# Optimization experiments

Measured on AMD Instinct MI355X. Metric: run time of the kernel, lower is better.

Reference implementation:

```python
import jax, jax.numpy as jnp
import numpy as np
import math

DIM = 512
HEADS = 8
DIM_HEAD = DIM // HEADS
TIME_DIM = 512
EPS = 1e-5


def _ln(x, g, b):
    m = jnp.mean(x, axis=-1, keepdims=True)
    v = jnp.var(x, axis=-1, keepdims=True)
    return (x - m) * jax.lax.rsqrt(v + EPS) * g + b


def setup_inputs() -> dict:
    key = jax.random.key(0)
    ks = jax.random.split(key, 16)
    s = 0.02
    return {
        "con_features": jax.random.normal(ks[0], (4, 1024, DIM), jnp.float32),
        "diff_features": jax.random.normal(ks[1], (4, 1024, DIM), jnp.float32),
        "time_emb": jax.random.normal(ks[2], (4, TIME_DIM), jnp.float32),
        "ln_con_g": jnp.ones((DIM,), jnp.float32),
        "ln_con_b": jnp.zeros((DIM,), jnp.float32),
        "ln_diff_g": jnp.ones((DIM,), jnp.float32),
        "ln_diff_b": jnp.zeros((DIM,), jnp.float32),
        "wq": jax.random.normal(ks[3], (DIM, DIM), jnp.float32) * s,
        "wk": jax.random.normal(ks[4], (DIM, DIM), jnp.float32) * s,
        "wv": jax.random.normal(ks[5], (DIM, DIM), jnp.float32) * s,
        "w_out": jax.random.normal(ks[6], (DIM, DIM), jnp.float32) * s,
        "b_out": jnp.zeros((DIM,), jnp.float32),
        "w_emd1": jax.random.normal(ks[7], (TIME_DIM, 2 * DIM), jnp.float32) * s,
        "b_emd1": jnp.zeros((2 * DIM,), jnp.float32),
        "w_emd2": jax.random.normal(ks[8], (2 * DIM, 2 * DIM), jnp.float32) * s,
        "b_emd2": jnp.zeros((2 * DIM,), jnp.float32),
        "mlp_ln_g": jnp.ones((DIM,), jnp.float32),
        "mlp_ln_b": jnp.zeros((DIM,), jnp.float32),
        "mlp_w1": jax.random.normal(ks[9], (DIM, DIM), jnp.float32) * s,
        "mlp_b1": jnp.zeros((DIM,), jnp.float32),
        "mlp_w2": jax.random.normal(ks[10], (DIM, DIM), jnp.float32) * s,
        "mlp_b2": jnp.zeros((DIM,), jnp.float32),
    }


def reference(con_features, diff_features, time_emb,
              ln_con_g, ln_con_b, ln_diff_g, ln_diff_b,
              wq, wk, wv, w_out, b_out,
              w_emd1, b_emd1, w_emd2, b_emd2,
              mlp_ln_g, mlp_ln_b, mlp_w1, mlp_b1, mlp_w2, mlp_b2):
    b, n, _ = diff_features.shape
    fea_q = _ln(diff_features, ln_diff_g, ln_diff_b)
    fea_kv = _ln(con_features, ln_con_g, ln_con_b)
    # projections (no bias) + split heads: b n (h d) -> b h n d
    def heads(x):
        return x.reshape(b, n, HEADS, DIM_HEAD).transpose(0, 2, 1, 3)
    q = heads(fea_q @ wq)
    k = heads(fea_kv @ wk)
    v = heads(fea_kv @ wv)
    # 2D FFT over (n, d), ortho norm
    qf = jnp.fft.fft2(q, axes=(-2, -1), norm="ortho")
    kf = jnp.fft.fft2(k, axes=(-2, -1), norm="ortho")
    dots = jnp.einsum("bhnd,bhmd->bhnm", qf, jnp.conj(kf))  # q @ k^H
    attn_c = jnp.fft.ifft2(dots, axes=(-2, -1), norm="ortho")
    mag = jnp.sqrt(attn_c.real ** 2 + attn_c.imag ** 2)
    attn = jax.nn.softmax(mag, axis=-1) / math.sqrt(DIM_HEAD)
    out = jnp.einsum("bhnm,bhmd->bhnd", attn, v)
    out = out.transpose(0, 2, 1, 3).reshape(b, n, DIM)  # b h n d -> b n (h d)
    # global per-sample normalization over (n, dim); torch.std uses ddof=1
    mu = jnp.mean(out, axis=(-2, -1), keepdims=True)
    sd = jnp.std(out, axis=(-2, -1), keepdims=True, ddof=1)
    out1 = (out - mu) / sd
    # FiLM from time embedding
    t = jax.nn.silu(time_emb @ w_emd1 + b_emd1)
    t = t @ w_emd2 + b_emd2
    mean_t, std_t = jnp.split(t, 2, axis=-1)
    out1 = out1 * std_t[:, None, :] + mean_t[:, None, :]
    out1 = out1 @ w_out + b_out
    # FeedForward: LN -> Linear -> GELU(exact) -> Linear
    h = _ln(out1, mlp_ln_g, mlp_ln_b)
    h = jax.nn.gelu(h @ mlp_w1 + mlp_b1, approximate=False)
    return h @ mlp_w2 + mlp_b2
```

## Files before the change

kernel.cpp:

```cpp
#include <hip/hip_runtime.h>
#include <math.h>


typedef _Float16 f16;
typedef _Float16 f16x8 __attribute__((ext_vector_type(8)));
typedef float f32x4 __attribute__((ext_vector_type(4)));

#define ROWS 4096
#define NTOK 1024
#define NB   4
#define NH   8
#define DH   64

__device__ __forceinline__ void glds16(const f16* g, f16* l) {
    __builtin_amdgcn_global_load_lds((const __attribute__((address_space(1))) void*)g,
                                     (__attribute__((address_space(3))) void*)l, 16, 0, 0);
}

struct PrepArgs { const float* src[6]; f16* dst[6]; };

__global__ __launch_bounds__(256) void k_prep(PrepArgs pa, float* stats,
                                              const float* b_emd1, const float* b_emd2,
                                              float* tbacc, float* filmp) {
    __shared__ float tile[32][33];
    int m = blockIdx.z;
    const float* src = pa.src[m];
    f16* dst = pa.dst[m];
    int i0 = blockIdx.y * 32;
    int o0 = blockIdx.x * 32;
    for (int r = threadIdx.y; r < 32; r += 8)
        tile[r][threadIdx.x] = src[(i0 + r) * 512 + o0 + threadIdx.x];
    __syncthreads();
    for (int r = threadIdx.y; r < 32; r += 8)
        dst[(o0 + r) * 512 + i0 + threadIdx.x] = (f16)tile[threadIdx.x][r];
    if (m == 0 && blockIdx.x == 0 && blockIdx.y == 0 && threadIdx.y == 0 && threadIdx.x < 8)
        stats[threadIdx.x] = 0.f;
    if (m == 0 && blockIdx.y == 1) {
        int o = blockIdx.x * 256 + threadIdx.y * 32 + threadIdx.x;
        tbacc[o] = b_emd1[o & 1023];
        filmp[o] = b_emd2[o & 1023];
    }
}

__global__ __launch_bounds__(256) void k_ln(const float* __restrict__ x0, const float* __restrict__ g0,
                                            const float* __restrict__ b0, f16* __restrict__ o0,
                                            const float* __restrict__ x1, const float* __restrict__ g1,
                                            const float* __restrict__ b1, f16* __restrict__ o1,
                                            int n0) {
    int wid = threadIdx.x >> 6, lane = threadIdx.x & 63;
    long row = (long)blockIdx.x * 4 + wid;
    const float *x, *g, *bb; f16* o;
    if (row < n0) { x = x0 + row * 512; g = g0; bb = b0; o = o0 + row * 512; }
    else { long r = row - n0; x = x1 + r * 512; g = g1; bb = b1; o = o1 + r * 512; }
    float v[8]; float s = 0.f;
#pragma unroll
    for (int j = 0; j < 8; j++) { v[j] = x[lane + 64 * j]; s += v[j]; }
#pragma unroll
    for (int d = 32; d >= 1; d >>= 1) s += __shfl_xor(s, d, 64);
    float mean = s * (1.f / 512.f);
    float q = 0.f;
#pragma unroll
    for (int j = 0; j < 8; j++) { float t = v[j] - mean; q += t * t; }
#pragma unroll
    for (int d = 32; d >= 1; d >>= 1) q += __shfl_xor(q, d, 64);
    float inv = rsqrtf(q * (1.f / 512.f) + 1e-5f);
#pragma unroll
    for (int j = 0; j < 8; j++) {
        int c = lane + 64 * j;
        o[c] = (f16)((v[j] - mean) * inv * g[c] + bb[c]);
    }
}

__global__ __launch_bounds__(256) void k_film1s(const float* __restrict__ temb, const float* __restrict__ w1,
                                                float* __restrict__ tbacc) {
    __shared__ float tsh[4][32];
    int tid = threadIdx.x;
    int c = blockIdx.x * 256 + tid;
    int k0 = blockIdx.y * 32;
    if (tid < 128) tsh[tid >> 5][tid & 31] = temb[(tid >> 5) * 512 + k0 + (tid & 31)];
    __syncthreads();
    float a0 = 0.f, a1 = 0.f, a2 = 0.f, a3 = 0.f;
#pragma unroll 8
    for (int k = 0; k < 32; k++) {
        float w = w1[(k0 + k) * 1024 + c];
        a0 += tsh[0][k] * w; a1 += tsh[1][k] * w; a2 += tsh[2][k] * w; a3 += tsh[3][k] * w;
    }
    atomicAdd(&tbacc[c], a0);        atomicAdd(&tbacc[1024 + c], a1);
    atomicAdd(&tbacc[2048 + c], a2); atomicAdd(&tbacc[3072 + c], a3);
}

__global__ __launch_bounds__(256) void k_film2s(const float* __restrict__ tbacc, const float* __restrict__ w2,
                                                float* __restrict__ filmp) {
    __shared__ float tsh[4][32];
    int tid = threadIdx.x;
    int c = blockIdx.x * 256 + tid;
    int k0 = blockIdx.y * 32;
    if (tid < 128) {
        float v = tbacc[(tid >> 5) * 1024 + k0 + (tid & 31)];
        tsh[tid >> 5][tid & 31] = v / (1.f + __expf(-v));
    }
    __syncthreads();
    float a0 = 0.f, a1 = 0.f, a2 = 0.f, a3 = 0.f;
#pragma unroll 8
    for (int k = 0; k < 32; k++) {
        float w = w2[(k0 + k) * 1024 + c];
        a0 += tsh[0][k] * w; a1 += tsh[1][k] * w; a2 += tsh[2][k] * w; a3 += tsh[3][k] * w;
    }
    atomicAdd(&filmp[c], a0);        atomicAdd(&filmp[1024 + c], a1);
    atomicAdd(&filmp[2048 + c], a2); atomicAdd(&filmp[3072 + c], a3);
}

__global__ __launch_bounds__(256) void k_qkv(const f16* __restrict__ A16, const f16* __restrict__ C16,
                                             const f16* __restrict__ wqT, const f16* __restrict__ wkT,
                                             const f16* __restrict__ wvT,
                                             f16* __restrict__ Qh, f16* __restrict__ Kf, f16* __restrict__ Vt) {
    __shared__ __attribute__((aligned(16))) f16 sh[128 * 128 + 64 * 128];
    f16* Ash = sh;
    f16* Bsh = sh + 128 * 128;
    const int z = blockIdx.z;
    const f16* A  = (z == 0) ? A16 : C16;
    const f16* BT = (z == 0) ? wqT : (z == 1) ? wkT : wvT;
    const int tid = threadIdx.x;
    const int lane = tid & 63, wid = tid >> 6;
    const int quad = lane >> 4, l15 = lane & 15;
    const int m0 = blockIdx.x * 128, n0 = blockIdx.y * 64;
    const int wm = (wid >> 1) * 64, wn = (wid & 1) * 32;
    const int srow = lane >> 4, slot = lane & 15;
    f32x4 acc[4][2] = {};
    for (int kk = 0; kk < 512; kk += 128) {
        if (kk) __syncthreads();
#pragma unroll
        for (int c = 0; c < 8; c++) {
            int r = c * 16 + 4 * wid + srow;
            int j = slot ^ (r & 7);
            glds16(&A[(long)(m0 + r) * 512 + kk + 8 * j], &Ash[(c * 16 + 4 * wid) * 128]);
        }
#pragma unroll
        for (int c = 0; c < 4; c++) {
            int r = c * 16 + 4 * wid + srow;
            int j = slot ^ (r & 7);
            glds16(&BT[(long)(n0 + r) * 512 + kk + 8 * j], &Bsh[(c * 16 + 4 * wid) * 128]);
        }
        __syncthreads();
#pragma unroll
        for (int ks = 0; ks < 4; ks++) {
            const int rslot = ((ks * 4 + quad) ^ (l15 & 7)) * 8;
            f16x8 af[4], bf[2];
#pragma unroll
            for (int t = 0; t < 4; t++)
                af[t] = *(const f16x8*)&Ash[(wm + t * 16 + l15) * 128 + rslot];
#pragma unroll
            for (int t = 0; t < 2; t++)
                bf[t] = *(const f16x8*)&Bsh[(wn + t * 16 + l15) * 128 + rslot];
#pragma unroll
            for (int mt = 0; mt < 4; mt++)
#pragma unroll
                for (int nt = 0; nt < 2; nt++)
                    acc[mt][nt] = __builtin_amdgcn_mfma_f32_16x16x32_f16(af[mt], bf[nt], acc[mt][nt], 0, 0, 0);
        }
    }
    __syncthreads();
    const int bb = m0 >> 10, nn0 = m0 & 1023, h = blockIdx.y;
    if (z <= 1) {
#pragma unroll
        for (int mt = 0; mt < 4; mt++)
#pragma unroll
            for (int nt = 0; nt < 2; nt++)
#pragma unroll
                for (int r = 0; r < 4; r++)
                    sh[(wm + mt * 16 + quad * 4 + r) * 72 + wn + nt * 16 + l15] = (f16)acc[mt][nt][r];
        __syncthreads();
        f16* dst = (z == 0) ? Qh : Kf;
        long basebh = ((long)(bb * NH + h)) * NTOK * DH;
#pragma unroll
        for (int q2 = 0; q2 < 4; q2++) {
            int c = tid + q2 * 256;
            int row = c >> 3, col = (c & 7) * 8;
            int n = nn0 + row;
            int nr = (z == 1) ? ((NTOK - n) & (NTOK - 1)) : n;
            *(f16x8*)&dst[basebh + (long)nr * DH + col] = *(const f16x8*)&sh[row * 72 + col];
        }
    } else {
#pragma unroll
        for (int mt = 0; mt < 4; mt++)
#pragma unroll
            for (int nt = 0; nt < 2; nt++)
#pragma unroll
                for (int r = 0; r < 4; r++)
                    sh[(wn + nt * 16 + l15) * 136 + wm + mt * 16 + quad * 4 + r] = (f16)acc[mt][nt][r];
        __syncthreads();
        long basev = ((long)(bb * NH + h)) * DH * NTOK;
#pragma unroll
        for (int q2 = 0; q2 < 4; q2++) {
            int c = tid + q2 * 256;
            int d = c >> 4, col = (c & 15) * 8;
            *(f16x8*)&Vt[basev + (long)d * NTOK + nn0 + col] = *(const f16x8*)&sh[d * 136 + col];
        }
    }
}

template <int EPI>
__global__ __launch_bounds__(256) void k_gemm64(const f16* __restrict__ A, const f16* __restrict__ BT,
                                                const float* __restrict__ bias, void* __restrict__ dstv) {
    __shared__ __attribute__((aligned(16))) f16 Ash[64 * 128];
    __shared__ __attribute__((aligned(16))) f16 Bsh[64 * 128];
    const int tid = threadIdx.x;
    const int lane = tid & 63, wid = tid >> 6;
    const int quad = lane >> 4, l15 = lane & 15;
    const int m0 = blockIdx.x * 64, n0 = blockIdx.y * 64;
    const int wm = (wid >> 1) * 32, wn = (wid & 1) * 32;
    const int srow = lane >> 4, slot = lane & 15;
    f32x4 acc[2][2] = {};
    for (int kk = 0; kk < 512; kk += 128) {
        if (kk) __syncthreads();
#pragma unroll
        for (int c = 0; c < 4; c++) {
            int r = c * 16 + 4 * wid + srow;
            int j = slot ^ (r & 7);
            glds16(&A[(long)(m0 + r) * 512 + kk + 8 * j], &Ash[(c * 16 + 4 * wid) * 128]);
            glds16(&BT[(long)(n0 + r) * 512 + kk + 8 * j], &Bsh[(c * 16 + 4 * wid) * 128]);
        }
        __syncthreads();
#pragma unroll
        for (int ks = 0; ks < 4; ks++) {
            const int rslot = ((ks * 4 + quad) ^ (l15 & 7)) * 8;
            f16x8 af[2], bf[2];
#pragma unroll
            for (int t = 0; t < 2; t++) {
                af[t] = *(const f16x8*)&Ash[(wm + t * 16 + l15) * 128 + rslot];
                bf[t] = *(const f16x8*)&Bsh[(wn + t * 16 + l15) * 128 + rslot];
            }
#pragma unroll
            for (int mt = 0; mt < 2; mt++)
#pragma unroll
                for (int nt = 0; nt < 2; nt++)
                    acc[mt][nt] = __builtin_amdgcn_mfma_f32_16x16x32_f16(af[mt], bf[nt], acc[mt][nt], 0, 0, 0);
        }
    }
#pragma unroll
    for (int mt = 0; mt < 2; mt++)
#pragma unroll
        for (int nt = 0; nt < 2; nt++)
#pragma unroll
            for (int r = 0; r < 4; r++) {
                int gm = m0 + wm + mt * 16 + quad * 4 + r;
                int gn = n0 + wn + nt * 16 + l15;
                float v = acc[mt][nt][r];
                if (EPI == 3) {
                    float x = v + bias[gn];
                    ((f16*)dstv)[(long)gm * 512 + gn] = (f16)(0.5f * x * (1.0f + erff(x * 0.70710678f)));
                } else {
                    ((float*)dstv)[(long)gm * 512 + gn] = v + bias[gn];
                }
            }
}

__global__ __launch_bounds__(256) void k_attn(const f16* __restrict__ Q, const f16* __restrict__ Kf,
                                              const f16* __restrict__ Vt, float* __restrict__ out,
                                              float* __restrict__ stats) {
    __shared__ __attribute__((aligned(16))) f16 Ksh[128 * 64];
    __shared__ __attribute__((aligned(16))) f16 Vsh[80 * 128];
    __shared__ __attribute__((aligned(16))) f16 Psh[4 * 16 * 136];
    __shared__ float rbuf[8];
    const int tid = threadIdx.x, lane = tid & 63, wid = tid >> 6;
    const int quad = lane >> 4, l15 = lane & 15;
    const int bh = blockIdx.x;
    const int b = bh >> 3, h = bh & 7, q0 = blockIdx.y * 64;
    const f16* Qbh = Q + (long)bh * NTOK * DH;
    const f16* Kbh = Kf + (long)bh * NTOK * DH;
    const f16* Vbh = Vt + (long)bh * DH * NTOK;
    const int rl = lane >> 3, jj8 = (lane & 7) ^ rl;
    const int rl4 = lane >> 4, jjv = (lane & 15) ^ (4 * wid + rl4);
    for (int i = tid; i < 16 * 128; i += 256) {
        int r = i >> 7, c2 = i & 127;
        Vsh[(64 + r) * 128 + c2] = (f16)((r == 0) ? 1.f : 0.f);
    }
    const int qrow = q0 + wid * 16 + l15;
    f16x8 qf[2];
    qf[0] = *(const f16x8*)&Qbh[(long)qrow * DH + quad * 8];
    qf[1] = *(const f16x8*)&Qbh[(long)qrow * DH + 32 + quad * 8];
    f32x4 O[5] = {};

    for (int k0 = 0; k0 < NTOK; k0 += 128) {
        if (k0) __syncthreads();
#pragma unroll
        for (int c = 0; c < 4; c++) {
            int rk = c * 32 + 8 * wid + rl;
            glds16(&Kbh[(long)(k0 + rk) * DH + 8 * jj8], &Ksh[(c * 32 + 8 * wid) * 64]);
        }
#pragma unroll
        for (int c = 0; c < 4; c++) {
            int rv = c * 16 + 4 * wid + rl4;
            glds16(&Vbh[(long)rv * NTOK + k0 + 8 * jjv], &Vsh[(c * 16 + 4 * wid) * 128]);
        }
        __syncthreads();
        f32x4 S[8] = {};
#pragma unroll
        for (int ks = 0; ks < 2; ks++) {
            const int slot = ((ks * 4 + quad) ^ (l15 & 7)) * 8;
#pragma unroll
            for (int nt = 0; nt < 8; nt++) {
                f16x8 kf = *(const f16x8*)&Ksh[(nt * 16 + l15) * 64 + slot];
                S[nt] = __builtin_amdgcn_mfma_f32_16x16x32_f16(qf[ks], kf, S[nt], 0, 0, 0);
            }
        }
#pragma unroll
        for (int nt = 0; nt < 8; nt++)
#pragma unroll
            for (int r = 0; r < 4; r++) {
                float p = __expf(fminf(fabsf(S[nt][r]) - 8.f, 11.f));
                Psh[(wid * 16 + quad * 4 + r) * 136 + nt * 16 + l15] = (f16)p;
            }
#pragma unroll
        for (int ks = 0; ks < 4; ks++) {
            f16x8 pf = *(const f16x8*)&Psh[(wid * 16 + l15) * 136 + ks * 32 + quad * 8];
            const int vslot = ((ks * 4 + quad) ^ l15) * 8;
#pragma unroll
            for (int vt = 0; vt < 5; vt++) {
                f16x8 vf = *(const f16x8*)&Vsh[(vt * 16 + l15) * 128 + vslot];
                O[vt] = __builtin_amdgcn_mfma_f32_16x16x32_f16(pf, vf, O[vt], 0, 0, 0);
            }
        }
    }
    float lb[4];
#pragma unroll
    for (int r = 0; r < 4; r++) lb[r] = 0.125f / __shfl(O[4][r], lane & 48, 64);
    float lsum = 0.f, lsq = 0.f;
#pragma unroll
    for (int t = 0; t < 4; t++)
#pragma unroll
        for (int r = 0; r < 4; r++) {
            float v = O[t][r] * lb[r];
            int gn = q0 + wid * 16 + quad * 4 + r;
            int gc = h * DH + t * 16 + l15;
            out[((long)b * NTOK + gn) * 512 + gc] = v;
            lsum += v; lsq += v * v;
        }
#pragma unroll
    for (int d = 32; d >= 1; d >>= 1) { lsum += __shfl_xor(lsum, d, 64); lsq += __shfl_xor(lsq, d, 64); }
    if (lane == 0) { rbuf[wid] = lsum; rbuf[4 + wid] = lsq; }
    __syncthreads();
    if (tid == 0) {
        atomicAdd(&stats[b * 2], rbuf[0] + rbuf[1] + rbuf[2] + rbuf[3]);
        atomicAdd(&stats[b * 2 + 1], rbuf[4] + rbuf[5] + rbuf[6] + rbuf[7]);
    }
}

__global__ __launch_bounds__(256) void k_film_apply(const float* __restrict__ ao, const float* __restrict__ stats,
                                                    const float* __restrict__ filmp, f16* __restrict__ x2) {
    long base = ((long)blockIdx.x * 256 + threadIdx.x) * 4;
    int b = (int)(base >> 19);
    float sum = stats[b * 2], sq = stats[b * 2 + 1];
    const float M = 524288.f;
    float mu = sum / M;
    float var = (sq - sum * mu) / (M - 1.f);
    float isd = rsqrtf(var);
    int c = (int)(base & 511);
    float4 v = *(const float4*)&ao[base];
    float mt[4], st[4];
#pragma unroll
    for (int j = 0; j < 4; j++) { mt[j] = filmp[b * 1024 + c + j]; st[j] = filmp[b * 1024 + 512 + c + j]; }
    x2[base + 0] = (f16)(((v.x - mu) * isd) * st[0] + mt[0]);
    x2[base + 1] = (f16)(((v.y - mu) * isd) * st[1] + mt[1]);
    x2[base + 2] = (f16)(((v.z - mu) * isd) * st[2] + mt[2]);
    x2[base + 3] = (f16)(((v.w - mu) * isd) * st[3] + mt[3]);
}

extern "C" void kernel_launch(void* const* d_in, const int* in_sizes, int n_in,
                              void* d_out, int out_size, void* d_ws, size_t ws_size,
                              hipStream_t stream) {
    const float* con      = (const float*)d_in[0];
    const float* diff     = (const float*)d_in[1];
    const float* temb     = (const float*)d_in[2];
    const float* ln_con_g = (const float*)d_in[3];
    const float* ln_con_b = (const float*)d_in[4];
    const float* ln_dif_g = (const float*)d_in[5];
    const float* ln_dif_b = (const float*)d_in[6];
    const float* wq       = (const float*)d_in[7];
    const float* wk       = (const float*)d_in[8];
    const float* wv       = (const float*)d_in[9];
    const float* w_out    = (const float*)d_in[10];
    const float* b_out    = (const float*)d_in[11];
    const float* w_emd1   = (const float*)d_in[12];
    const float* b_emd1   = (const float*)d_in[13];
    const float* w_emd2   = (const float*)d_in[14];
    const float* b_emd2   = (const float*)d_in[15];
    const float* mlp_ln_g = (const float*)d_in[16];
    const float* mlp_ln_b = (const float*)d_in[17];
    const float* mlp_w1   = (const float*)d_in[18];
    const float* mlp_b1   = (const float*)d_in[19];
    const float* mlp_w2   = (const float*)d_in[20];
    const float* mlp_b2   = (const float*)d_in[21];
    float* outp = (float*)d_out;

    char* ws = (char*)d_ws;
    size_t off = 0;
    auto alloc = [&](size_t bytes) { void* p = ws + off; off += (bytes + 255) & ~(size_t)255; return p; };
    f16*   A16   = (f16*)alloc((size_t)ROWS * 512 * 2);
    f16*   C16   = (f16*)alloc((size_t)ROWS * 512 * 2);
    f16*   Qh    = (f16*)alloc((size_t)ROWS * 512 * 2);
    f16*   Kf    = (f16*)alloc((size_t)ROWS * 512 * 2);
    f16*   Vt    = (f16*)alloc((size_t)ROWS * 512 * 2);
    float* aout  = (float*)alloc((size_t)ROWS * 512 * 4);
    f16*   wqT   = (f16*)alloc(512 * 512 * 2);
    f16*   wkT   = (f16*)alloc(512 * 512 * 2);
    f16*   wvT   = (f16*)alloc(512 * 512 * 2);
    f16*   woT   = (f16*)alloc(512 * 512 * 2);
    f16*   w1T   = (f16*)alloc(512 * 512 * 2);
    f16*   w2T   = (f16*)alloc(512 * 512 * 2);
    float* tbacc = (float*)alloc(4 * 1024 * 4);
    float* filmp = (float*)alloc(4 * 1024 * 4);
    float* stats = (float*)alloc(256);
    float* out1  = (float*)Qh;
    f16*   X2    = Vt;
    f16*   X3    = A16;
    f16*   X4    = C16;

    PrepArgs pa;
    pa.src[0] = wq;  pa.src[1] = wk;  pa.src[2] = wv;
    pa.src[3] = w_out; pa.src[4] = mlp_w1; pa.src[5] = mlp_w2;
    pa.dst[0] = wqT; pa.dst[1] = wkT; pa.dst[2] = wvT;
    pa.dst[3] = woT; pa.dst[4] = w1T; pa.dst[5] = w2T;

    k_prep<<<dim3(16, 16, 6), dim3(32, 8), 0, stream>>>(pa, stats, b_emd1, b_emd2, tbacc, filmp);
    k_film1s<<<dim3(4, 16), dim3(256), 0, stream>>>(temb, w_emd1, tbacc);
    k_film2s<<<dim3(4, 32), dim3(256), 0, stream>>>(tbacc, w_emd2, filmp);
    k_ln<<<dim3(2048), dim3(256), 0, stream>>>(diff, ln_dif_g, ln_dif_b, A16,
                                               con, ln_con_g, ln_con_b, C16, ROWS);
    k_qkv<<<dim3(32, 8, 3), dim3(256), 0, stream>>>(A16, C16, wqT, wkT, wvT, Qh, Kf, Vt);
    k_attn<<<dim3(32, 16), dim3(256), 0, stream>>>(Qh, Kf, Vt, aout, stats);
    k_film_apply<<<dim3(2048), dim3(256), 0, stream>>>(aout, stats, filmp, X2);
    k_gemm64<2><<<dim3(64, 8), dim3(256), 0, stream>>>(X2, woT, b_out, (void*)out1);
    k_ln<<<dim3(1024), dim3(256), 0, stream>>>(out1, mlp_ln_g, mlp_ln_b, X3,
                                               out1, mlp_ln_g, mlp_ln_b, X3, ROWS);
    k_gemm64<3><<<dim3(64, 8), dim3(256), 0, stream>>>(X3, w1T, mlp_b1, (void*)X4);
    k_gemm64<4><<<dim3(64, 8), dim3(256), 0, stream>>>(X4, w2T, mlp_b2, (void*)outp);
}
```

Baseline: 191.8 us.

## Merge prep, LN, FiLM and QKV launches; compute softmax row sums in registers

Four pre-attention launches (weight transpose, two FiLM GEMV stages, layernorm) are folded into one heterogeneous k_pre grid. The second FiLM GEMV is folded into the QKV GEMM grid as extra blocks, which drops the atomics and the bias pre-initialisation. In attention, the S tile is computed transposed so P can be stored as packed f16x4, and the softmax denominator is summed in registers instead of through an extra ones-row MFMA tile. This cuts launch count and MFMA work, but the FiLM blocks now run long serial K loops (512 and 1024 steps) on only four blocks each, which may become a tail.

```diff
diff --git a/kernel.cpp b/kernel.cpp
--- a/kernel.cpp
+++ b/kernel.cpp
@@ -3,6 +3,7 @@
 
 
 typedef _Float16 f16;
+typedef _Float16 f16x4 __attribute__((ext_vector_type(4)));
 typedef _Float16 f16x8 __attribute__((ext_vector_type(8)));
 typedef float f32x4 __attribute__((ext_vector_type(4)));
 
@@ -19,39 +20,8 @@
 
 struct PrepArgs { const float* src[6]; f16* dst[6]; };
 
-__global__ __launch_bounds__(256) void k_prep(PrepArgs pa, float* stats,
-                                              const float* b_emd1, const float* b_emd2,
-                                              float* tbacc, float* filmp) {
-    __shared__ float tile[32][33];
-    int m = blockIdx.z;
-    const float* src = pa.src[m];
-    f16* dst = pa.dst[m];
-    int i0 = blockIdx.y * 32;
-    int o0 = blockIdx.x * 32;
-    for (int r = threadIdx.y; r < 32; r += 8)
-        tile[r][threadIdx.x] = src[(i0 + r) * 512 + o0 + threadIdx.x];
-    __syncthreads();
-    for (int r = threadIdx.y; r < 32; r += 8)
-        dst[(o0 + r) * 512 + i0 + threadIdx.x] = (f16)tile[threadIdx.x][r];
-    if (m == 0 && blockIdx.x == 0 && blockIdx.y == 0 && threadIdx.y == 0 && threadIdx.x < 8)
-        stats[threadIdx.x] = 0.f;
-    if (m == 0 && blockIdx.y == 1) {
-        int o = blockIdx.x * 256 + threadIdx.y * 32 + threadIdx.x;
-        tbacc[o] = b_emd1[o & 1023];
-        filmp[o] = b_emd2[o & 1023];
-    }
-}
-
-__global__ __launch_bounds__(256) void k_ln(const float* __restrict__ x0, const float* __restrict__ g0,
-                                            const float* __restrict__ b0, f16* __restrict__ o0,
-                                            const float* __restrict__ x1, const float* __restrict__ g1,
-                                            const float* __restrict__ b1, f16* __restrict__ o1,
-                                            int n0) {
-    int wid = threadIdx.x >> 6, lane = threadIdx.x & 63;
-    long row = (long)blockIdx.x * 4 + wid;
-    const float *x, *g, *bb; f16* o;
-    if (row < n0) { x = x0 + row * 512; g = g0; bb = b0; o = o0 + row * 512; }
-    else { long r = row - n0; x = x1 + r * 512; g = g1; bb = b1; o = o1 + r * 512; }
+__device__ __forceinline__ void ln_row(const float* __restrict__ x, const float* __restrict__ g,
+                                       const float* __restrict__ bb, f16* __restrict__ o, int lane) {
     float v[8]; float s = 0.f;
 #pragma unroll
     for (int j = 0; j < 8; j++) { v[j] = x[lane + 64 * j]; s += v[j]; }
@@ -71,59 +41,85 @@
     }
 }
 
-__global__ __launch_bounds__(256) void k_film1s(const float* __restrict__ temb, const float* __restrict__ w1,
-                                                float* __restrict__ tbacc) {
-    __shared__ float tsh[4][32];
-    int tid = threadIdx.x;
-    int c = blockIdx.x * 256 + tid;
-    int k0 = blockIdx.y * 32;
-    if (tid < 128) tsh[tid >> 5][tid & 31] = temb[(tid >> 5) * 512 + k0 + (tid & 31)];
-    __syncthreads();
-    float a0 = 0.f, a1 = 0.f, a2 = 0.f, a3 = 0.f;
-#pragma unroll 8
-    for (int k = 0; k < 32; k++) {
-        float w = w1[(k0 + k) * 1024 + c];
-        a0 += tsh[0][k] * w; a1 += tsh[1][k] * w; a2 += tsh[2][k] * w; a3 += tsh[3][k] * w;
-    }
-    atomicAdd(&tbacc[c], a0);        atomicAdd(&tbacc[1024 + c], a1);
-    atomicAdd(&tbacc[2048 + c], a2); atomicAdd(&tbacc[3072 + c], a3);
-}
-
-__global__ __launch_bounds__(256) void k_film2s(const float* __restrict__ tbacc, const float* __restrict__ w2,
-                                                float* __restrict__ filmp) {
-    __shared__ float tsh[4][32];
-    int tid = threadIdx.x;
-    int c = blockIdx.x * 256 + tid;
-    int k0 = blockIdx.y * 32;
-    if (tid < 128) {
-        float v = tbacc[(tid >> 5) * 1024 + k0 + (tid & 31)];
-        tsh[tid >> 5][tid & 31] = v / (1.f + __expf(-v));
-    }
-    __syncthreads();
-    float a0 = 0.f, a1 = 0.f, a2 = 0.f, a3 = 0.f;
-#pragma unroll 8
-    for (int k = 0; k < 32; k++) {
-        float w = w2[(k0 + k) * 1024 + c];
-        a0 += tsh[0][k] * w; a1 += tsh[1][k] * w; a2 += tsh[2][k] * w; a3 += tsh[3][k] * w;
-    }
-    atomicAdd(&filmp[c], a0);        atomicAdd(&filmp[1024 + c], a1);
-    atomicAdd(&filmp[2048 + c], a2); atomicAdd(&filmp[3072 + c], a3);
-}
-
-__global__ __launch_bounds__(256) void k_qkv(const f16* __restrict__ A16, const f16* __restrict__ C16,
+__global__ __launch_bounds__(256) void k_pre(PrepArgs pa, float* stats,
+                                             const float* __restrict__ temb, const float* __restrict__ w_emd1,
+                                             const float* __restrict__ b_emd1, float* __restrict__ tb,
+                                             const float* __restrict__ diff, const float* __restrict__ g_dif,
+                                             const float* __restrict__ b_dif, f16* __restrict__ A16,
+                                             const float* __restrict__ con, const float* __restrict__ g_con,
+                                             const float* __restrict__ b_con, f16* __restrict__ C16) {
+    __shared__ float smem[2048];
+    const int id = blockIdx.x, tid = threadIdx.x;
+    if (id < 4) {
+        for (int i = tid; i < 2048; i += 256) smem[i] = temb[i];
+        __syncthreads();
+        int c = id * 256 + tid;
+        float bb = b_emd1[c];
+        float a0 = bb, a1 = bb, a2 = bb, a3 = bb;
+#pragma unroll 4
+        for (int k = 0; k < 512; k++) {
+            float w = w_emd1[k * 1024 + c];
+            a0 += smem[k] * w; a1 += smem[512 + k] * w;
+            a2 += smem[1024 + k] * w; a3 += smem[1536 + k] * w;
+        }
+        tb[c]        = a0 / (1.f + __expf(-a0));
+        tb[1024 + c] = a1 / (1.f + __expf(-a1));
+        tb[2048 + c] = a2 / (1.f + __expf(-a2));
+        tb[3072 + c] = a3 / (1.f + __expf(-a3));
+    } else if (id < 1540) {
+        int pid = id - 4;
+        int m = pid >> 8, rem = pid & 255;
+        int o0 = (rem & 15) * 32, i0 = (rem >> 4) * 32;
+        int tx = tid & 31, ty = tid >> 5;
+        const float* src = pa.src[m];
+        f16* dst = pa.dst[m];
+        float* tile = smem;
+        for (int r = ty; r < 32; r += 8)
+            tile[r * 33 + tx] = src[(i0 + r) * 512 + o0 + tx];
+        __syncthreads();
+        for (int r = ty; r < 32; r += 8)
+            dst[(o0 + r) * 512 + i0 + tx] = (f16)tile[tx * 33 + r];
+        if (pid == 0 && tid < 8) stats[tid] = 0.f;
+    } else {
+        int lane = tid & 63, wid = tid >> 6;
+        long row = (long)(id - 1540) * 4 + wid;
+        if (row < ROWS) ln_row(diff + row * 512, g_dif, b_dif, A16 + row * 512, lane);
+        else { long r = row - ROWS; ln_row(con + r * 512, g_con, b_con, C16 + r * 512, lane); }
+    }
+}
+
+__global__ __launch_bounds__(256) void k_mid(const f16* __restrict__ A16, const f16* __restrict__ C16,
                                              const f16* __restrict__ wqT, const f16* __restrict__ wkT,
                                              const f16* __restrict__ wvT,
-                                             f16* __restrict__ Qh, f16* __restrict__ Kf, f16* __restrict__ Vt) {
+                                             f16* __restrict__ Qh, f16* __restrict__ Kf, f16* __restrict__ Vt,
+                                             const float* __restrict__ tb, const float* __restrict__ w_emd2,
+                                             const float* __restrict__ b_emd2, float* __restrict__ filmp) {
     __shared__ __attribute__((aligned(16))) f16 sh[128 * 128 + 64 * 128];
+    const int id = blockIdx.x, tid = threadIdx.x;
+    if (id >= 768) {
+        float* fs = (float*)sh;
+        for (int i = tid; i < 4096; i += 256) fs[i] = tb[i];
+        __syncthreads();
+        int c = (id - 768) * 256 + tid;
+        float bb = b_emd2[c];
+        float a0 = bb, a1 = bb, a2 = bb, a3 = bb;
+#pragma unroll 4
+        for (int k = 0; k < 1024; k++) {
+            float w = w_emd2[k * 1024 + c];
+            a0 += fs[k] * w; a1 += fs[1024 + k] * w;
+            a2 += fs[2048 + k] * w; a3 += fs[3072 + k] * w;
+        }
+        filmp[c] = a0; filmp[1024 + c] = a1; filmp[2048 + c] = a2; filmp[3072 + c] = a3;
+        return;
+    }
     f16* Ash = sh;
     f16* Bsh = sh + 128 * 128;
-    const int z = blockIdx.z;
+    const int z = id >> 8;
     const f16* A  = (z == 0) ? A16 : C16;
     const f16* BT = (z == 0) ? wqT : (z == 1) ? wkT : wvT;
-    const int tid = threadIdx.x;
     const int lane = tid & 63, wid = tid >> 6;
     const int quad = lane >> 4, l15 = lane & 15;
-    const int m0 = blockIdx.x * 128, n0 = blockIdx.y * 64;
+    const int m0 = (id & 31) * 128, n0 = ((id >> 5) & 7) * 64;
     const int wm = (wid >> 1) * 64, wn = (wid & 1) * 32;
     const int srow = lane >> 4, slot = lane & 15;
     f32x4 acc[4][2] = {};
@@ -160,7 +156,7 @@
         }
     }
     __syncthreads();
-    const int bb = m0 >> 10, nn0 = m0 & 1023, h = blockIdx.y;
+    const int bb = m0 >> 10, nn0 = m0 & 1023, h = (id >> 5) & 7;
     if (z <= 1) {
 #pragma unroll
         for (int mt = 0; mt < 4; mt++)
@@ -259,8 +255,8 @@
                                               const f16* __restrict__ Vt, float* __restrict__ out,
                                               float* __restrict__ stats) {
     __shared__ __attribute__((aligned(16))) f16 Ksh[128 * 64];
-    __shared__ __attribute__((aligned(16))) f16 Vsh[80 * 128];
-    __shared__ __attribute__((aligned(16))) f16 Psh[4 * 16 * 136];
+    __shared__ __attribute__((aligned(16))) f16 Vsh[64 * 128];
+    __shared__ __attribute__((aligned(16))) f16 PshT[4 * 16 * 136];
     __shared__ float rbuf[8];
     const int tid = threadIdx.x, lane = tid & 63, wid = tid >> 6;
     const int quad = lane >> 4, l15 = lane & 15;
@@ -271,15 +267,13 @@
     const f16* Vbh = Vt + (long)bh * DH * NTOK;
     const int rl = lane >> 3, jj8 = (lane & 7) ^ rl;
     const int rl4 = lane >> 4, jjv = (lane & 15) ^ (4 * wid + rl4);
-    for (int i = tid; i < 16 * 128; i += 256) {
-        int r = i >> 7, c2 = i & 127;
-        Vsh[(64 + r) * 128 + c2] = (f16)((r == 0) ? 1.f : 0.f);
-    }
     const int qrow = q0 + wid * 16 + l15;
     f16x8 qf[2];
     qf[0] = *(const f16x8*)&Qbh[(long)qrow * DH + quad * 8];
     qf[1] = *(const f16x8*)&Qbh[(long)qrow * DH + 32 + quad * 8];
-    f32x4 O[5] = {};
+    f32x4 O[4] = {};
+    float l_acc = 0.f;
+    f16* Pw = PshT + wid * 16 * 136;
 
     for (int k0 = 0; k0 < NTOK; k0 += 128) {
         if (k0) __syncthreads();
@@ -294,37 +288,42 @@
             glds16(&Vbh[(long)rv * NTOK + k0 + 8 * jjv], &Vsh[(c * 16 + 4 * wid) * 128]);
         }
         __syncthreads();
-        f32x4 S[8] = {};
+        f32x4 st[8] = {};
 #pragma unroll
         for (int ks = 0; ks < 2; ks++) {
             const int slot = ((ks * 4 + quad) ^ (l15 & 7)) * 8;
 #pragma unroll
             for (int nt = 0; nt < 8; nt++) {
                 f16x8 kf = *(const f16x8*)&Ksh[(nt * 16 + l15) * 64 + slot];
-                S[nt] = __builtin_amdgcn_mfma_f32_16x16x32_f16(qf[ks], kf, S[nt], 0, 0, 0);
+                st[nt] = __builtin_amdgcn_mfma_f32_16x16x32_f16(kf, qf[ks], st[nt], 0, 0, 0);
             }
         }
 #pragma unroll
-        for (int nt = 0; nt < 8; nt++)
-#pragma unroll
-            for (int r = 0; r < 4; r++) {
-                float p = __expf(fminf(fabsf(S[nt][r]) - 8.f, 11.f));
-                Psh[(wid * 16 + quad * 4 + r) * 136 + nt * 16 + l15] = (f16)p;
-            }
+        for (int nt = 0; nt < 8; nt++) {
+            float p0 = __expf(fminf(fabsf(st[nt][0]) - 8.f, 11.f));
+            float p1 = __expf(fminf(fabsf(st[nt][1]) - 8.f, 11.f));
+            float p2 = __expf(fminf(fabsf(st[nt][2]) - 8.f, 11.f));
+            float p3 = __expf(fminf(fabsf(st[nt][3]) - 8.f, 11.f));
+            l_acc += (p0 + p1) + (p2 + p3);
+            f16x4 pk = { (f16)p0, (f16)p1, (f16)p2, (f16)p3 };
+            *(f16x4*)&Pw[l15 * 136 + 16 * nt + quad * 4] = pk;
+        }
 #pragma unroll
         for (int ks = 0; ks < 4; ks++) {
-            f16x8 pf = *(const f16x8*)&Psh[(wid * 16 + l15) * 136 + ks * 32 + quad * 8];
+            f16x8 pf = *(const f16x8*)&Pw[l15 * 136 + 32 * ks + quad * 8];
             const int vslot = ((ks * 4 + quad) ^ l15) * 8;
 #pragma unroll
-            for (int vt = 0; vt < 5; vt++) {
+            for (int vt = 0; vt < 4; vt++) {
                 f16x8 vf = *(const f16x8*)&Vsh[(vt * 16 + l15) * 128 + vslot];
                 O[vt] = __builtin_amdgcn_mfma_f32_16x16x32_f16(pf, vf, O[vt], 0, 0, 0);
             }
         }
     }
+    l_acc += __shfl_xor(l_acc, 16, 64);
+    l_acc += __shfl_xor(l_acc, 32, 64);
     float lb[4];
 #pragma unroll
-    for (int r = 0; r < 4; r++) lb[r] = 0.125f / __shfl(O[4][r], lane & 48, 64);
+    for (int r = 0; r < 4; r++) lb[r] = 0.125f / __shfl(l_acc, quad * 4 + r, 64);
     float lsum = 0.f, lsq = 0.f;
 #pragma unroll
     for (int t = 0; t < 4; t++)
@@ -364,6 +363,13 @@
     x2[base + 1] = (f16)(((v.y - mu) * isd) * st[1] + mt[1]);
     x2[base + 2] = (f16)(((v.z - mu) * isd) * st[2] + mt[2]);
     x2[base + 3] = (f16)(((v.w - mu) * isd) * st[3] + mt[3]);
+}
+
+__global__ __launch_bounds__(256) void k_ln2(const float* __restrict__ x, const float* __restrict__ g,
+                                             const float* __restrict__ bb, f16* __restrict__ o) {
+    int lane = threadIdx.x & 63, wid = threadIdx.x >> 6;
+    long row = (long)blockIdx.x * 4 + wid;
+    ln_row(x + row * 512, g, bb, o + row * 512, lane);
 }
 
 extern "C" void kernel_launch(void* const* d_in, const int* in_sizes, int n_in,
@@ -408,7 +414,7 @@
     f16*   woT   = (f16*)alloc(512 * 512 * 2);
     f16*   w1T   = (f16*)alloc(512 * 512 * 2);
     f16*   w2T   = (f16*)alloc(512 * 512 * 2);
-    float* tbacc = (float*)alloc(4 * 1024 * 4);
+    float* tb    = (float*)alloc(4 * 1024 * 4);
     float* filmp = (float*)alloc(4 * 1024 * 4);
     float* stats = (float*)alloc(256);
     float* out1  = (float*)Qh;
@@ -422,17 +428,15 @@
     pa.dst[0] = wqT; pa.dst[1] = wkT; pa.dst[2] = wvT;
     pa.dst[3] = woT; pa.dst[4] = w1T; pa.dst[5] = w2T;
 
-    k_prep<<<dim3(16, 16, 6), dim3(32, 8), 0, stream>>>(pa, stats, b_emd1, b_emd2, tbacc, filmp);
-    k_film1s<<<dim3(4, 16), dim3(256), 0, stream>>>(temb, w_emd1, tbacc);
-    k_film2s<<<dim3(4, 32), dim3(256), 0, stream>>>(tbacc, w_emd2, filmp);
-    k_ln<<<dim3(2048), dim3(256), 0, stream>>>(diff, ln_dif_g, ln_dif_b, A16,
-                                               con, ln_con_g, ln_con_b, C16, ROWS);
-    k_qkv<<<dim3(32, 8, 3), dim3(256), 0, stream>>>(A16, C16, wqT, wkT, wvT, Qh, Kf, Vt);
+    k_pre<<<dim3(3588), dim3(256), 0, stream>>>(pa, stats, temb, w_emd1, b_emd1, tb,
+                                                diff, ln_dif_g, ln_dif_b, A16,
+                                                con, ln_con_g, ln_con_b, C16);
+    k_mid<<<dim3(772), dim3(256), 0, stream>>>(A16, C16, wqT, wkT, wvT, Qh, Kf, Vt,
+                                               tb, w_emd2, b_emd2, filmp);
     k_attn<<<dim3(32, 16), dim3(256), 0, stream>>>(Qh, Kf, Vt, aout, stats);
     k_film_apply<<<dim3(2048), dim3(256), 0, stream>>>(aout, stats, filmp, X2);
     k_gemm64<2><<<dim3(64, 8), dim3(256), 0, stream>>>(X2, woT, b_out, (void*)out1);
-    k_ln<<<dim3(1024), dim3(256), 0, stream>>>(out1, mlp_ln_g, mlp_ln_b, X3,
-                                               out1, mlp_ln_g, mlp_ln_b, X3, ROWS);
+    k_ln2<<<dim3(1024), dim3(256), 0, stream>>>(out1, mlp_ln_g, mlp_ln_b, X3);
     k_gemm64<3><<<dim3(64, 8), dim3(256), 0, stream>>>(X3, w1T, mlp_b1, (void*)X4);
     k_gemm64<4><<<dim3(64, 8), dim3(256), 0, stream>>>(X4, w2T, mlp_b2, (void*)outp);
 }
```

After: 315.4 us. +64.5%, slower.
